# Kernel tuning notes

Hardware: AMD Instinct MI355X
Metric: run time of the kernel (lower is better)

Reference implementation:

```python
import jax, jax.numpy as jnp
import numpy as np

C_IN = 128
D_K = 256
D_V = 256
N_HEAD = 8
H = 192
W = 192
REGION = 3
TEMPER = int(np.sqrt(D_K))  # int(sqrt(d_k)) per the torch module


def setup_inputs() -> dict:
    key = jax.random.key(0)
    k1, k2, k3, k4 = jax.random.split(key, 4)
    scale = 1.0 / np.sqrt(C_IN).astype(np.float32)
    x = jax.random.normal(k1, (1, C_IN, H, W), dtype=jnp.float32)
    wq = jax.random.normal(k2, (D_K, C_IN), dtype=jnp.float32) * scale
    wk = jax.random.normal(k3, (D_K, C_IN), dtype=jnp.float32) * scale
    wv = jax.random.normal(k4, (D_V, C_IN), dtype=jnp.float32) * scale
    return {"x": x, "wq": wq, "wk": wk, "wv": wv}


def _stretch(t):
    # Equivalent of the fixed Conv3d 'stretch' trick: for each (i, j) in the
    # 3x3 region, channel 3*i+j holds the input shifted by (i-1, j-1), zero-padded.
    # t: [b, d, H, W] -> [b, 9, d, H, W]
    b, d, h, w = t.shape
    tp = jnp.pad(t, ((0, 0), (0, 0), (1, 1), (1, 1)))
    return jnp.stack(
        [tp[:, :, i:i + h, j:j + w] for i in range(REGION) for j in range(REGION)],
        axis=1,
    )


def reference(x, wq, wk, wv):
    b = x.shape[0]  # must be 1 (module's broadcast only works for batch 1)
    dkh = D_K // N_HEAD
    dvh = D_V // N_HEAD
    r2 = REGION * REGION
    # 1x1 conv projections == channel matmuls
    q = jnp.einsum('oc,bchw->bohw', wq, x)
    k = jnp.einsum('oc,bchw->bohw', wk, x)
    v = jnp.einsum('oc,bchw->bohw', wv, x)
    Q = _stretch(q)  # [b, 9, d_k, H, W]
    K = _stretch(k)
    V = _stretch(v)  # [b, 9, d_v, H, W]
    # elementwise QK, per-head channel sum, scale, softmax over the 9 region slots
    qk = (Q * K).reshape(b, r2, N_HEAD, dkh, H, W)
    scores = jax.nn.softmax(qk.sum(axis=3) / TEMPER, axis=1)  # [b, 9, n_head, H, W]
    # dropout is identity in eval mode (att_drop disabled for the reference)
    Vh = V.reshape(b, r2, N_HEAD, dvh, H, W)
    out = (scores[:, :, :, None] * Vh).sum(axis=1).reshape(b, D_V, H, W)
    return out
```

## Files before the change

### kernel.cpp

```cpp
#include <hip/hip_runtime.h>

#define HW_   36864
#define WI    192
#define HT    192
#define CIN   128
#define DK    256
#define NH    8
#define DKH   32

using short4_ = __attribute__((ext_vector_type(4))) short;
using short8  = __attribute__((ext_vector_type(8))) short;
using float4_ = __attribute__((ext_vector_type(4))) float;

static __device__ __forceinline__ float b2f(unsigned short u) {
    union { unsigned int i; float f; } x; x.i = ((unsigned int)u) << 16; return x.f;
}
static __device__ __forceinline__ unsigned short f2b(float f) {
    union { float f; unsigned int i; } x; x.f = f;
    unsigned int r = x.i + 0x7FFFu + ((x.i >> 16) & 1u);
    return (unsigned short)(r >> 16);
}

__global__ __launch_bounds__(256) void convw_kernel(
    const float* __restrict__ wq,
    const float* __restrict__ wk,
    const float* __restrict__ wv,
    unsigned short* __restrict__ wqkv)
{
    int id = blockIdx.x * 256 + threadIdx.x;
    int h   = id / 12288;
    int rem = id - h * 12288;
    int r   = rem >> 7;
    int c   = rem & 127;
    int g   = r >> 4;
    int gm  = g % 3;
    int rr  = ((g >= 3) ? 16 : 0) + (r & 15);
    const float* __restrict__ s = (gm == 0) ? wq : ((gm == 1) ? wk : wv);
    wqkv[id] = f2b(s[(h * 32 + rr) * 128 + c]);
}

__global__ __launch_bounds__(256) void fusedattn_kernel(
    const float* __restrict__ x,
    const unsigned short* __restrict__ wqkv,
    float* __restrict__ out)
{
    __shared__ __align__(16) unsigned short Bs[208 * 136];
    __shared__ __align__(16) unsigned short Vt[208 * 40];
    __shared__ float Sc[2][208];

    const int blk   = blockIdx.x;
    const int hbase = (blk & 1) * 4;
    const int tile  = blk >> 1;
    const int ty = tile >> 3, tx = tile & 7;
    const int y0 = ty * 6, x0 = tx * 24;
    const int t    = threadIdx.x;
    const int lane = t & 63, wave = t >> 6;
    const int col  = lane & 15, quad = lane >> 4;
    const int wm   = wave >> 1, wn = wave & 1;
    const int ntb  = wn * 6;

    short8 a[3][4];
    {
        const unsigned short* __restrict__ Ag = wqkv + hbase * 12288;
        #pragma unroll
        for (int mt = 0; mt < 3; ++mt)
            #pragma unroll
            for (int kt = 0; kt < 4; ++kt)
                a[mt][kt] = *(const short8*)&Ag[(wm * 48 + mt * 16 + col) * 128 + kt * 32 + quad * 8];
    }

    if (t < 208) {
        int hy = t / 26, hx = t - hy * 26;
        int gy = y0 - 1 + hy; gy = gy < 0 ? 0 : (gy > HT - 1 ? HT - 1 : gy);
        int gx = x0 - 1 + hx; gx = gx < 0 ? 0 : (gx > WI - 1 ? WI - 1 : gx);
        const float* __restrict__ xp = x + gy * WI + gx;
        unsigned short* bp = Bs + t * 136;
        #pragma unroll 8
        for (int c = 0; c < 128; ++c)
            bp[c] = f2b(xp[(size_t)c * HW_]);
    }
    __syncthreads();

    for (int hh = 0; hh < 4; ++hh) {
        const int head = hbase + hh;

        float4_ acc[3][7];
        #pragma unroll
        for (int mt = 0; mt < 3; ++mt)
            #pragma unroll
            for (int j = 0; j < 7; ++j)
                acc[mt][j] = (float4_){0.f, 0.f, 0.f, 0.f};

        #pragma unroll
        for (int j = 0; j < 7; ++j) {
            const int p = (ntb + j) * 16 + col;
            short8 bb[4];
            #pragma unroll
            for (int kt = 0; kt < 4; ++kt)
                bb[kt] = *(const short8*)&Bs[p * 136 + kt * 32 + quad * 8];
            #pragma unroll
            for (int mt = 0; mt < 3; ++mt)
                #pragma unroll
                for (int kt = 0; kt < 4; ++kt)
                    acc[mt][j] = __builtin_amdgcn_mfma_f32_16x16x32_bf16(a[mt][kt], bb[kt], acc[mt][j], 0, 0, 0);
        }

        if (hh < 3) {
            const unsigned short* __restrict__ Ag = wqkv + (head + 1) * 12288;
            #pragma unroll
            for (int mt = 0; mt < 3; ++mt)
                #pragma unroll
                for (int kt = 0; kt < 4; ++kt)
                    a[mt][kt] = *(const short8*)&Ag[(wm * 48 + mt * 16 + col) * 128 + kt * 32 + quad * 8];
        }

        #pragma unroll
        for (int j = 0; j < 7; ++j) {
            const int p = (ntb + j) * 16 + col;
            float s = 0.f;
            #pragma unroll
            for (int reg = 0; reg < 4; ++reg)
                s += acc[0][j][reg] * acc[1][j][reg];
            s += __shfl_xor(s, 16, 64);
            s += __shfl_xor(s, 32, 64);
            if (quad == 0) Sc[wm][p] = s;
            short4_ v0;
            #pragma unroll
            for (int reg = 0; reg < 4; ++reg)
                v0[reg] = (short)f2b(acc[2][j][reg]);
            *(short4_*)&Vt[p * 40 + wm * 16 + quad * 4] = v0;
        }
        __syncthreads();

        for (int idx = t; idx < 288; idx += 256) {
            const int pxl = idx >> 1;
            const int hg  = idx & 1;
            const int ly  = pxl / 24, lx = pxl - ly * 24;
            const int y   = y0 + ly, xx = x0 + lx;

            float w[9];
            float m = -1e30f;
            #pragma unroll
            for (int r = 0; r < 9; ++r) {
                int dy = r / 3 - 1, dx = r % 3 - 1;
                int ny = y + dy, nx = xx + dx;
                bool inb = (ny >= 0) && (ny < HT) && (nx >= 0) && (nx < WI);
                int hp = (ly + 1 + dy) * 26 + lx + 1 + dx;
                float val = inb ? ((Sc[0][hp] + Sc[1][hp]) * 0.0625f) : 0.0f;
                w[r] = val;
                m = fmaxf(m, val);
            }
            float wsum = 0.f;
            #pragma unroll
            for (int r = 0; r < 9; ++r) {
                float e = __expf(w[r] - m);
                w[r] = e;
                wsum += e;
            }
            float inv = 1.0f / wsum;
            #pragma unroll
            for (int r = 0; r < 9; ++r) {
                int dy = r / 3 - 1, dx = r % 3 - 1;
                int ny = y + dy, nx = xx + dx;
                bool inb = (ny >= 0) && (ny < HT) && (nx >= 0) && (nx < WI);
                w[r] = inb ? (w[r] * inv) : 0.0f;
            }

            float o[16];
            #pragma unroll
            for (int j2 = 0; j2 < 16; ++j2) o[j2] = 0.f;
            #pragma unroll
            for (int r = 0; r < 9; ++r) {
                int dy = r / 3 - 1, dx = r % 3 - 1;
                int hp = (ly + 1 + dy) * 26 + lx + 1 + dx;
                const unsigned short* vp = &Vt[hp * 40 + hg * 16];
                short8 v8a = *(const short8*)&vp[0];
                short8 v8b = *(const short8*)&vp[8];
                #pragma unroll
                for (int j2 = 0; j2 < 8; ++j2) {
                    o[j2]     = fmaf(w[r], b2f((unsigned short)v8a[j2]), o[j2]);
                    o[8 + j2] = fmaf(w[r], b2f((unsigned short)v8b[j2]), o[8 + j2]);
                }
            }
            float* op = out + (size_t)(head * DKH + hg * 16) * HW_ + y * WI + xx;
            #pragma unroll
            for (int j2 = 0; j2 < 16; ++j2)
                op[(size_t)j2 * HW_] = o[j2];
        }
        __syncthreads();
    }
}

extern "C" void kernel_launch(void* const* d_in, const int* in_sizes, int n_in,
                              void* d_out, int out_size, void* d_ws, size_t ws_size,
                              hipStream_t stream) {
    const float* x  = (const float*)d_in[0];
    const float* wq = (const float*)d_in[1];
    const float* wk = (const float*)d_in[2];
    const float* wv = (const float*)d_in[3];

    unsigned short* wqkv = (unsigned short*)d_ws;

    convw_kernel<<<384, 256, 0, stream>>>(wq, wk, wv, wqkv);
    fusedattn_kernel<<<512, 256, 0, stream>>>(x, wqkv, (float*)d_out);
}
```

Baseline: 117.1 us.

## Shrink spatial tile to 16x4 with more blocks and XCD-aware block remap

Changes the spatial tile from 24x6 to 16x4 pixels, so the grid grows from 512 to 1152 blocks and LDS use per block drops, giving higher occupancy and better balance across CUs. All 256 threads now do the softmax/aggregation step, each handling one pixel and 8 channels, where before 288 work items were spread over 256 threads with a ragged second pass. The halo load is split across two thread groups by channel parity, and the block index is remapped so neighbouring tiles land on the same XCD. The trade-off is more halo overhead (108 halo pixels for 64 outputs, against 208 for 144), so there is more redundant projection MFMA work and more x reads per output.

```diff
diff --git a/kernel.cpp b/kernel.cpp
--- a/kernel.cpp
+++ b/kernel.cpp
@@ -7,6 +7,14 @@
 #define DK    256
 #define NH    8
 #define DKH   32
+
+#define TW    16
+#define TH    4
+#define HWH   18
+#define HHH   6
+#define HPX   108
+#define HPAD  112
+#define VTS   36
 
 using short4_ = __attribute__((ext_vector_type(4))) short;
 using short8  = __attribute__((ext_vector_type(8))) short;
@@ -39,25 +47,26 @@
     wqkv[id] = f2b(s[(h * 32 + rr) * 128 + c]);
 }
 
-__global__ __launch_bounds__(256) void fusedattn_kernel(
+__global__ __launch_bounds__(256) void fusedattn2_kernel(
     const float* __restrict__ x,
     const unsigned short* __restrict__ wqkv,
     float* __restrict__ out)
 {
-    __shared__ __align__(16) unsigned short Bs[208 * 136];
-    __shared__ __align__(16) unsigned short Vt[208 * 40];
-    __shared__ float Sc[2][208];
-
-    const int blk   = blockIdx.x;
-    const int hbase = (blk & 1) * 4;
-    const int tile  = blk >> 1;
-    const int ty = tile >> 3, tx = tile & 7;
-    const int y0 = ty * 6, x0 = tx * 24;
+    __shared__ __align__(16) unsigned short Bs[HPAD * 136];
+    __shared__ __align__(16) unsigned short Vt[HPAD * VTS];
+    __shared__ float Sc[2][HPAD];
+
+    const int b    = blockIdx.x;
+    const int wg   = (b & 7) * 144 + (b >> 3);
+    const int hbase = (wg & 1) * 4;
+    const int tile  = wg >> 1;
+    const int ty = tile / 12, tx = tile - ty * 12;
+    const int y0 = ty * TH, x0 = tx * TW;
+
     const int t    = threadIdx.x;
     const int lane = t & 63, wave = t >> 6;
     const int col  = lane & 15, quad = lane >> 4;
     const int wm   = wave >> 1, wn = wave & 1;
-    const int ntb  = wn * 6;
 
     short8 a[3][4];
     {
@@ -69,31 +78,37 @@
                 a[mt][kt] = *(const short8*)&Ag[(wm * 48 + mt * 16 + col) * 128 + kt * 32 + quad * 8];
     }
 
-    if (t < 208) {
-        int hy = t / 26, hx = t - hy * 26;
-        int gy = y0 - 1 + hy; gy = gy < 0 ? 0 : (gy > HT - 1 ? HT - 1 : gy);
-        int gx = x0 - 1 + hx; gx = gx < 0 ? 0 : (gx > WI - 1 ? WI - 1 : gx);
-        const float* __restrict__ xp = x + gy * WI + gx;
-        unsigned short* bp = Bs + t * 136;
-        #pragma unroll 8
-        for (int c = 0; c < 128; ++c)
-            bp[c] = f2b(xp[(size_t)c * HW_]);
+    {
+        const int p  = t & 127;
+        const int cb = t >> 7;
+        if (p < HPX) {
+            int hy = p / HWH, hx = p - hy * HWH;
+            int gy = y0 - 1 + hy; gy = gy < 0 ? 0 : (gy > HT - 1 ? HT - 1 : gy);
+            int gx = x0 - 1 + hx; gx = gx < 0 ? 0 : (gx > WI - 1 ? WI - 1 : gx);
+            const float* __restrict__ xp = x + gy * WI + gx;
+            unsigned short* __restrict__ bp = Bs + p * 136;
+            #pragma unroll 8
+            for (int i = 0; i < 64; ++i) {
+                int c = cb + 2 * i;
+                bp[c] = f2b(xp[(size_t)c * HW_]);
+            }
+        }
     }
     __syncthreads();
 
     for (int hh = 0; hh < 4; ++hh) {
         const int head = hbase + hh;
 
-        float4_ acc[3][7];
+        float4_ acc[3][4];
         #pragma unroll
         for (int mt = 0; mt < 3; ++mt)
             #pragma unroll
-            for (int j = 0; j < 7; ++j)
+            for (int j = 0; j < 4; ++j)
                 acc[mt][j] = (float4_){0.f, 0.f, 0.f, 0.f};
 
         #pragma unroll
-        for (int j = 0; j < 7; ++j) {
-            const int p = (ntb + j) * 16 + col;
+        for (int j = 0; j < 4; ++j) {
+            const int p = (wn * 3 + j) * 16 + col;
             short8 bb[4];
             #pragma unroll
             for (int kt = 0; kt < 4; ++kt)
@@ -115,8 +130,8 @@
         }
 
         #pragma unroll
-        for (int j = 0; j < 7; ++j) {
-            const int p = (ntb + j) * 16 + col;
+        for (int j = 0; j < 4; ++j) {
+            const int p = (wn * 3 + j) * 16 + col;
             float s = 0.f;
             #pragma unroll
             for (int reg = 0; reg < 4; ++reg)
@@ -128,14 +143,14 @@
             #pragma unroll
             for (int reg = 0; reg < 4; ++reg)
                 v0[reg] = (short)f2b(acc[2][j][reg]);
-            *(short4_*)&Vt[p * 40 + wm * 16 + quad * 4] = v0;
+            *(short4_*)&Vt[p * VTS + wm * 16 + quad * 4] = v0;
         }
         __syncthreads();
 
-        for (int idx = t; idx < 288; idx += 256) {
-            const int pxl = idx >> 1;
-            const int hg  = idx & 1;
-            const int ly  = pxl / 24, lx = pxl - ly * 24;
+        {
+            const int pxl = t >> 2;
+            const int cg  = t & 3;
+            const int ly  = pxl >> 4, lx = pxl & 15;
             const int y   = y0 + ly, xx = x0 + lx;
 
             float w[9];
@@ -145,7 +160,7 @@
                 int dy = r / 3 - 1, dx = r % 3 - 1;
                 int ny = y + dy, nx = xx + dx;
                 bool inb = (ny >= 0) && (ny < HT) && (nx >= 0) && (nx < WI);
-                int hp = (ly + 1 + dy) * 26 + lx + 1 + dx;
+                int hp = (ly + 1 + dy) * HWH + lx + 1 + dx;
                 float val = inb ? ((Sc[0][hp] + Sc[1][hp]) * 0.0625f) : 0.0f;
                 w[r] = val;
                 m = fmaxf(m, val);
@@ -166,25 +181,24 @@
                 w[r] = inb ? (w[r] * inv) : 0.0f;
             }
 
-            float o[16];
-            #pragma unroll
-            for (int j2 = 0; j2 < 16; ++j2) o[j2] = 0.f;
+            float o[8];
+            #pragma unroll
+            for (int j2 = 0; j2 < 8; ++j2) o[j2] = 0.f;
             #pragma unroll
             for (int r = 0; r < 9; ++r) {
                 int dy = r / 3 - 1, dx = r % 3 - 1;
-                int hp = (ly + 1 + dy) * 26 + lx + 1 + dx;
-                const unsigned short* vp = &Vt[hp * 40 + hg * 16];
-                short8 v8a = *(const short8*)&vp[0];
-                short8 v8b = *(const short8*)&vp[8];
+                int hp = (ly + 1 + dy) * HWH + lx + 1 + dx;
+                short4_ va = *(const short4_*)&Vt[hp * VTS + cg * 8];
+                short4_ vb = *(const short4_*)&Vt[hp * VTS + cg * 8 + 4];
                 #pragma unroll
-                for (int j2 = 0; j2 < 8; ++j2) {
-                    o[j2]     = fmaf(w[r], b2f((unsigned short)v8a[j2]), o[j2]);
-                    o[8 + j2] = fmaf(w[r], b2f((unsigned short)v8b[j2]), o[8 + j2]);
+                for (int j2 = 0; j2 < 4; ++j2) {
+                    o[j2]     = fmaf(w[r], b2f((unsigned short)va[j2]), o[j2]);
+                    o[4 + j2] = fmaf(w[r], b2f((unsigned short)vb[j2]), o[4 + j2]);
                 }
             }
-            float* op = out + (size_t)(head * DKH + hg * 16) * HW_ + y * WI + xx;
-            #pragma unroll
-            for (int j2 = 0; j2 < 16; ++j2)
+            float* op = out + (size_t)(head * DKH + cg * 8) * HW_ + y * WI + xx;
+            #pragma unroll
+            for (int j2 = 0; j2 < 8; ++j2)
                 op[(size_t)j2 * HW_] = o[j2];
         }
         __syncthreads();
@@ -202,5 +216,5 @@
     unsigned short* wqkv = (unsigned short*)d_ws;
 
     convw_kernel<<<384, 256, 0, stream>>>(wq, wk, wv, wqkv);
-    fusedattn_kernel<<<512, 256, 0, stream>>>(x, wqkv, (float*)d_out);
-}
+    fusedattn2_kernel<<<1152, 256, 0, stream>>>(x, wqkv, (float*)d_out);
+}
```

Result: slower. 124.9 us (+6.7%).
